# Optimization experiments

Hardware: AMD Instinct MI355X
Metric: run time of the kernel (lower is better)

The kernel has to match this reference:

```python
import jax, jax.numpy as jnp
import numpy as np

EPS = 1e-12  # F.normalize default eps


def setup_inputs() -> dict:
    key = jax.random.key(0)
    x = jax.random.normal(key, (10000, 512), dtype=jnp.float32)
    return {"x": x, "k": 9}


def reference(x, k):
    # F.normalize(x, p=2, dim=0): L2-normalize each feature column over points
    col_norm = jnp.sqrt(jnp.sum(x * x, axis=0, keepdims=True))  # [1, D]
    xn = x / jnp.maximum(col_norm, EPS)                          # [N, D]

    # pairwise squared euclidean distance: ||xi||^2 - 2 xi.xj + ||xj||^2
    sq = jnp.sum(xn * xn, axis=-1, keepdims=True)                # [N, 1]
    dist = sq - 2.0 * (xn @ xn.T) + sq.T                          # [N, N]

    # k nearest neighbors = top-k of negative distance
    _, nn_idx = jax.lax.top_k(-dist, k)                           # [N, k] int32

    n = x.shape[0]
    center_idx = jnp.broadcast_to(jnp.arange(n, dtype=nn_idx.dtype)[:, None], (n, k))
    edge_idx = jnp.stack((nn_idx, center_idx), axis=0)            # [2, N, k]
    return edge_idx
```

## Files before the change

kernel.cpp:

```cpp
#include <hip/hip_runtime.h>
#include <hip/hip_cooperative_groups.h>
#include <math.h>

namespace cg = cooperative_groups;

#define DD 512
#define NBLKA 400

#define PM 128
#define PN 256
#define KB 32
#define CSPLIT 6
#define NC 12
#define PBUF 32
#define PBSTRIDE 36
#define NCTOT (CSPLIT*NC)
#define KOUTMAX 16
#define RS_MARGIN 2e-4f

typedef __attribute__((ext_vector_type(8))) short bf16x8;
typedef __attribute__((ext_vector_type(4))) float f32x4;

static __device__ __forceinline__ unsigned short f2bf(float f) {
    unsigned u = __float_as_uint(f);
    u += 0x7fff + ((u >> 16) & 1);
    return (unsigned short)(u >> 16);
}

__global__ __launch_bounds__(256) void prekernel(
    const float* __restrict__ x, double* __restrict__ partial,
    double* __restrict__ rn, double* __restrict__ w,
    double* __restrict__ sq, float* __restrict__ sqf,
    unsigned short* __restrict__ xnbf, int N, int rows_per_block, int nblk)
{
    cg::grid_group grid = cg::this_grid();
    const int t = threadIdx.x;

    {
        int b  = blockIdx.x;
        int r0 = b * rows_per_block;
        int r1 = min(r0 + rows_per_block, N);
        double s0 = 0.0, s1 = 0.0;
        for (int r = r0; r < r1; ++r) {
            float v0 = x[(size_t)r * DD + t];
            float v1 = x[(size_t)r * DD + t + 256];
            s0 += (double)v0 * (double)v0;
            s1 += (double)v1 * (double)v1;
        }
        partial[(size_t)b * DD + t]       = s0;
        partial[(size_t)b * DD + t + 256] = s1;
    }
    grid.sync();

    __shared__ double red[256];
    if (blockIdx.x < 256) {
#pragma unroll 1
        for (int cc = 0; cc < 2; ++cc) {
            int c = blockIdx.x * 2 + cc;
            double s = 0.0;
            for (int b = t; b < nblk; b += 256) s += partial[(size_t)b * DD + c];
            red[t] = s;
            __syncthreads();
            for (int off = 128; off > 0; off >>= 1) {
                if (t < off) red[t] += red[t + off];
                __syncthreads();
            }
            if (t == 0) {
                double n = fmax(sqrt(red[0]), 1e-12);
                double r = 1.0 / n;
                rn[c] = r;
                w[c]  = r * r;
            }
            __syncthreads();
        }
    }
    grid.sync();

    {
        int lane   = t & 63;
        int gwave  = (blockIdx.x * blockDim.x + t) >> 6;
        int nwaves = (gridDim.x * blockDim.x) >> 6;
        const double2* rp = (const double2*)rn;
        double2 r0a = rp[lane * 2],       r0b = rp[lane * 2 + 1];
        double2 r1a = rp[128 + lane * 2], r1b = rp[128 + lane * 2 + 1];
        for (int i = gwave; i < N; i += nwaves) {
            const float4* xr = (const float4*)(x + (size_t)i * DD);
            float4 v0 = xr[lane];
            float4 v1 = xr[64 + lane];
            double a0 = (double)v0.x * r0a.x, a1 = (double)v0.y * r0a.y;
            double a2 = (double)v0.z * r0b.x, a3 = (double)v0.w * r0b.y;
            double b0 = (double)v1.x * r1a.x, b1 = (double)v1.y * r1a.y;
            double b2 = (double)v1.z * r1b.x, b3 = (double)v1.w * r1b.y;
            ushort4 s0 = { f2bf((float)a0), f2bf((float)a1), f2bf((float)a2), f2bf((float)a3) };
            ushort4 s1 = { f2bf((float)b0), f2bf((float)b1), f2bf((float)b2), f2bf((float)b3) };
            *(ushort4*)(xnbf + (size_t)i * DD + lane * 4)       = s0;
            *(ushort4*)(xnbf + (size_t)i * DD + 256 + lane * 4) = s1;
            double loc = a0*a0 + a1*a1 + a2*a2 + a3*a3 + b0*b0 + b1*b1 + b2*b2 + b3*b3;
#pragma unroll
            for (int off = 32; off > 0; off >>= 1)
                loc += __shfl_xor(loc, off, 64);
            if (lane == 0) { sq[i] = loc; sqf[i] = (float)loc; }
        }
    }
}

__global__ __launch_bounds__(512, 2) void gemm_dummy_guard() {}

__global__ __launch_bounds__(256, 2) void gemm_prefilter(
    const unsigned short* __restrict__ xnbf,
    const float* __restrict__ sqf, int* __restrict__ cand, float* __restrict__ cands,
    int N, int ntileM, int ntileN)
{
    __shared__ __align__(16) unsigned char lds_raw[49152];
    __shared__ float sqi_s[PM];
    __shared__ float sqj_s[PN];
    __shared__ float thr_s[PM];
    __shared__ int   cnt_s[PM];
    __shared__ int   flag_s;

    float (*Bsc)[PBSTRIDE] = (float (*)[PBSTRIDE]) lds_raw;
    int   (*Bid)[PBSTRIDE] = (int   (*)[PBSTRIDE]) (lds_raw + 24576);

    const int bid   = blockIdx.x;
    const int q     = bid & 7;
    const int s     = bid >> 3;
    const int ridx  = s / CSPLIT;
    const int split = s - ridx * CSPLIT;
    const int rowb  = q + 8 * ridx;
    if (rowb >= ntileM) return;
    const int row0  = rowb * PM;

    const int t      = threadIdx.x;
    const int lane15 = t & 15;
    const int quad   = (t >> 4) & 3;
    const int wave   = t >> 6;
    const int wr     = (wave >> 1) * 64;
    const int wc     = (wave & 1) * 128;
    const int sl     = quad ^ (lane15 & 3);

    if (t == 0) flag_s = 0;
    if (t < PM) {
        int i = row0 + t;
        sqi_s[t] = (i < N) ? sqf[i] : 0.f;
        thr_s[t] = __builtin_inff();
        cnt_s[t] = 0;
    }

    float ls[NC];
    int   li[NC];
#pragma unroll
    for (int m = 0; m < NC; ++m) { ls[m] = __builtin_inff(); li[m] = 0x7fffffff; }

    f32x4 acc[4][8];

    for (int tile = split; tile < ntileN; tile += CSPLIT) {
        int col0 = tile * PN;

        {
            int j = col0 + t;
            sqj_s[t] = (j < N) ? sqf[j] : __builtin_inff();
        }
        __syncthreads();

#pragma unroll
        for (int mt = 0; mt < 4; ++mt)
#pragma unroll
            for (int nt = 0; nt < 8; ++nt)
                acc[mt][nt] = (f32x4){0.f, 0.f, 0.f, 0.f};

        auto STAGE = [&](int kc, int buf) {
            unsigned char* base = lds_raw + (size_t)buf * 24576;
#pragma unroll
            for (int l = 0; l < 2; ++l) {
                int e   = t + l * 256;
                int row = e >> 2;
                int c   = (e & 3) ^ (row & 3);
                size_t g = (size_t)(row0 + row) * DD + kc + c * 8;
                __builtin_amdgcn_global_load_lds(
                    (const unsigned int*)(xnbf + g),
                    (unsigned int*)(base + (size_t)e * 16), 16, 0, 0);
            }
#pragma unroll
            for (int l = 0; l < 4; ++l) {
                int e   = t + l * 256;
                int row = e >> 2;
                int c   = (e & 3) ^ (row & 3);
                size_t g = (size_t)(col0 + row) * DD + kc + c * 8;
                __builtin_amdgcn_global_load_lds(
                    (const unsigned int*)(xnbf + g),
                    (unsigned int*)(base + 8192 + (size_t)e * 16), 16, 0, 0);
            }
        };

        STAGE(0, 0);
#pragma unroll 1
        for (int cc = 0; cc < 16; ++cc) {
            if (cc < 15) {
                STAGE((cc + 1) * KB, (cc + 1) & 1);
                __builtin_amdgcn_sched_barrier(0);
                asm volatile("s_waitcnt vmcnt(6)" ::: "memory");
            } else {
                __builtin_amdgcn_sched_barrier(0);
                asm volatile("s_waitcnt vmcnt(0)" ::: "memory");
            }
            __builtin_amdgcn_s_barrier();
            __builtin_amdgcn_sched_barrier(0);

            const unsigned char* rb = lds_raw + (size_t)(cc & 1) * 24576;
            bf16x8 af[4], bfg[8];
#pragma unroll
            for (int mt = 0; mt < 4; ++mt)
                af[mt] = *(const bf16x8*)(rb + (size_t)(wr + mt * 16 + lane15) * 64 + sl * 16);
#pragma unroll
            for (int nt = 0; nt < 8; ++nt)
                bfg[nt] = *(const bf16x8*)(rb + 8192 + (size_t)(wc + nt * 16 + lane15) * 64 + sl * 16);
#pragma unroll
            for (int mt = 0; mt < 4; ++mt)
#pragma unroll
                for (int nt = 0; nt < 8; ++nt)
                    acc[mt][nt] = __builtin_amdgcn_mfma_f32_16x16x32_bf16(
                        af[mt], bfg[nt], acc[mt][nt], 0, 0, 0);
            __builtin_amdgcn_sched_barrier(0);
            __builtin_amdgcn_s_barrier();
        }

#pragma unroll
        for (int mt = 0; mt < 4; ++mt)
#pragma unroll
            for (int nt = 0; nt < 8; ++nt)
#pragma unroll
                for (int reg = 0; reg < 4; ++reg) {
                    int rl = wr + mt * 16 + quad * 4 + reg;
                    int cl = wc + nt * 16 + lane15;
                    float g = acc[mt][nt][reg];
                    acc[mt][nt][reg] = (sqi_s[rl] - 2.f * g) + sqj_s[cl];
                }
        __syncthreads();

        bool tile_edge = (col0 + PN > N);
        unsigned long long done0 = 0ull, done1 = 0ull;
        for (;;) {
#pragma unroll
            for (int hn = 0; hn < 2; ++hn) {
#pragma unroll
                for (int mt = 0; mt < 4; ++mt)
#pragma unroll
                    for (int reg = 0; reg < 4; ++reg) {
                        const unsigned long long gb =
                            (0x1111ull << reg) << (mt * 16);
                        unsigned long long dn = hn ? done1 : done0;
                        int rl = wr + mt * 16 + quad * 4 + reg;
                        float th = thr_s[rl];
                        float gmin = fminf(
                            fminf(acc[mt][hn * 4 + 0][reg], acc[mt][hn * 4 + 1][reg]),
                            fminf(acc[mt][hn * 4 + 2][reg], acc[mt][hn * 4 + 3][reg]));
                        if (!tile_edge && gmin > th) {
                            if (hn) done1 |= gb; else done0 |= gb;
                            continue;
                        }
                        if ((dn & gb) == gb) continue;
#pragma unroll
                        for (int u = 0; u < 4; ++u) {
                            const unsigned long long bit = 1ull << (mt * 16 + u * 4 + reg);
                            if (!(dn & bit)) {
                                float sv = acc[mt][hn * 4 + u][reg];
                                int   j  = col0 + wc + (hn * 4 + u) * 16 + lane15;
                                bool ok = false;
                                if (j < N && sv <= th) {
                                    int pos = atomicAdd(&cnt_s[rl], 1);
                                    if (pos < PBUF) {
                                        Bsc[rl][pos] = sv;
                                        Bid[rl][pos] = j;
                                        ok = true;
                                    }
                                } else {
                                    ok = true;
                                }
                                if (ok) { if (hn) done1 |= bit; else done0 |= bit; }
                            }
                        }
                    }
            }
            if (done0 != ~0ull || done1 != ~0ull) flag_s = 1;
            __syncthreads();
            if (t < PM) {
                int c = cnt_s[t];
                if (c > PBUF) c = PBUF;
                cnt_s[t] = 0;
                for (int m0 = 0; m0 < c; m0 += 4) {
                    float4 s4 = *(const float4*)&Bsc[t][m0];
                    int4   j4 = *(const int4*)&Bid[t][m0];
#pragma unroll
                    for (int e = 0; e < 4; ++e) {
                        if (m0 + e >= c) break;
                        float sv = (e == 0) ? s4.x : (e == 1) ? s4.y : (e == 2) ? s4.z : s4.w;
                        int   j  = (e == 0) ? j4.x : (e == 1) ? j4.y : (e == 2) ? j4.z : j4.w;
                        if (sv < ls[NC - 1] || (sv == ls[NC - 1] && j < li[NC - 1])) {
                            float cs = sv; int cj = j;
#pragma unroll
                            for (int p = 0; p < NC; ++p) {
                                bool lt = (cs < ls[p]) || (cs == ls[p] && cj < li[p]);
                                float ts = ls[p]; int tj = li[p];
                                if (lt) { ls[p] = cs; li[p] = cj; cs = ts; cj = tj; }
                            }
                        }
                    }
                }
                thr_s[t] = ls[NC - 1];
            }
            __syncthreads();
            int go = flag_s;
            __syncthreads();
            if (t == 0) flag_s = 0;
            __syncthreads();
            if (!go) break;
        }
    }
    if (t < PM) {
        int i = row0 + t;
        if (i < N) {
#pragma unroll
            for (int m = 0; m < NC; ++m) {
                cand [(size_t)i * NCTOT + split * NC + m] = li[m];
                cands[(size_t)i * NCTOT + split * NC + m] = ls[m];
            }
        }
    }
}

__global__ __launch_bounds__(256) void rescore_topk(
    const float* __restrict__ x, const double* __restrict__ w,
    const double* __restrict__ sq, const int* __restrict__ cand,
    const float* __restrict__ cands, int* __restrict__ out, int N, int k)
{
    __shared__ float Ssc[4][NCTOT];
    int lane = threadIdx.x & 63;
    int wid  = threadIdx.x >> 6;
    int i = blockIdx.x * 4 + wid;
    if (i >= N) return;

    size_t base = (size_t)i * NCTOT;
    Ssc[wid][lane] = cands[base + lane];
    if (lane < NCTOT - 64) Ssc[wid][64 + lane] = cands[base + 64 + lane];

    float p0 = Ssc[wid][lane];
    float p1 = Ssc[wid][64 + (lane & 7)];
    int c0 = 0, c1 = 0;
    for (int m = 0; m < NCTOT; ++m) {
        float s = Ssc[wid][m];
        c0 += (s <= p0); c1 += (s <= p1);
    }
    float best = __builtin_inff();
    if (c0 >= k) best = p0;
    if (c1 >= k && p1 < best) best = p1;
#pragma unroll
    for (int off = 32; off > 0; off >>= 1)
        best = fminf(best, __shfl_xor(best, off, 64));
    float cut = best + RS_MARGIN;

    double aw[8];
#pragma unroll
    for (int c = 0; c < 8; ++c) {
        int d = lane + 64 * c;
        aw[c] = (double)x[(size_t)i * DD + d] * w[d];
    }
    double sqi = sq[i];

    double bs[KOUTMAX];
    int    bj[KOUTMAX];
    for (int r = 0; r < k; ++r) { bs[r] = __builtin_inf(); bj[r] = 0x7fffffff; }

    int pend = -1;
    for (int m = 0; m <= NCTOT; ++m) {
        int j1cand = -1;
        if (m < NCTOT) {
            if (Ssc[wid][m] > cut) continue;
            j1cand = cand[base + m];
            if (pend < 0) { pend = j1cand; continue; }
        } else if (pend < 0) {
            break;
        }
        int j0 = pend, j1 = j1cand;
        pend = -1;
        const float* q0 = &x[(size_t)j0 * DD + lane];
        const float* q1 = (j1 >= 0) ? &x[(size_t)j1 * DD + lane] : q0;
        float v0[8], v1[8];
#pragma unroll
        for (int c = 0; c < 8; ++c) v0[c] = q0[64 * c];
#pragma unroll
        for (int c = 0; c < 8; ++c) v1[c] = q1[64 * c];
        double d0 = 0.0, d1 = 0.0;
#pragma unroll
        for (int c = 0; c < 8; ++c) d0 = fma(aw[c], (double)v0[c], d0);
#pragma unroll
        for (int c = 0; c < 8; ++c) d1 = fma(aw[c], (double)v1[c], d1);
#pragma unroll
        for (int off = 32; off > 0; off >>= 1) {
            d0 += __shfl_xor(d0, off, 64);
            d1 += __shfl_xor(d1, off, 64);
        }
        double s0 = (sqi - 2.0 * d0) + sq[j0];
        double s1 = (j1 >= 0) ? (sqi - 2.0 * d1) + sq[j1] : __builtin_inf();
#pragma unroll 1
        for (int pick = 0; pick < 2; ++pick) {
            double sv = pick ? s1 : s0;
            int    j  = pick ? j1 : j0;
            if (j < 0) continue;
            if (sv < bs[k - 1] || (sv == bs[k - 1] && j < bj[k - 1])) {
                int pos = k - 1;
                while (pos > 0) {
                    double ps = bs[pos - 1]; int pj = bj[pos - 1];
                    if (!(sv < ps || (sv == ps && j < pj))) break;
                    bs[pos] = ps; bj[pos] = pj;
                    --pos;
                }
                bs[pos] = sv; bj[pos] = j;
            }
        }
    }
    if (lane == 0) {
        for (int r = 0; r < k; ++r) {
            out[(size_t)i * k + r]                 = bj[r];
            out[(size_t)N * k + (size_t)i * k + r] = i;
        }
    }
}

extern "C" void kernel_launch(void* const* d_in, const int* in_sizes, int n_in,
                              void* d_out, int out_size, void* d_ws, size_t ws_size,
                              hipStream_t stream) {
    const float* x = (const float*)d_in[0];
    int N = in_sizes[0] / DD;
    int k = out_size / (2 * N);
    if (k > KOUTMAX) k = KOUTMAX;

    char* ws = (char*)d_ws;
    double*         partial = (double*)ws;
    double*         rn      = (double*)(ws + 1638400);
    double*         w       = (double*)(ws + 1642496);
    double*         sq      = (double*)(ws + 1646592);
    float*          sqf     = (float*) (ws + 1726592);
    unsigned short* xnbf    = (unsigned short*)(ws + 1766592);
    int*            cand    = (int*)   (ws + 12006592);
    float*          cands   = (float*) (ws + 14886592);

    int rpb  = (N + NBLKA - 1) / NBLKA;
    int nblk = NBLKA;
    void* pre_args[] = { (void*)&x, (void*)&partial, (void*)&rn, (void*)&w,
                         (void*)&sq, (void*)&sqf, (void*)&xnbf,
                         (void*)&N, (void*)&rpb, (void*)&nblk };
    hipLaunchCooperativeKernel((const void*)prekernel, dim3(NBLKA), dim3(256),
                               pre_args, 0, stream);

    int ntileM = (N + PM - 1) / PM;
    int ntileN = (N + PN - 1) / PN;
    int rows_per_xcd = (ntileM + 7) / 8;
    int nblkc = 8 * rows_per_xcd * CSPLIT;
    hipLaunchKernelGGL(gemm_prefilter, dim3(nblkc), dim3(256), 0, stream,
                       xnbf, sqf, cand, cands, N, ntileM, ntileN);

    hipLaunchKernelGGL(rescore_topk, dim3((N + 3) / 4), dim3(256), 0, stream,
                       x, w, sq, cand, cands, (int*)d_out, N, k);
}
```

Before: 712.1 us.

## Switch prefilter GEMM from bf16 to scaled fp8 MFMA with wider candidate set

Normalized features are quantized to e4m3 fp8 (scaled by 32) instead of bf16, and the prefilter GEMM uses the fp8 16x16x32 MFMA with K-chunks of 32 bytes, halving staging traffic and LDS use. Per-split candidate count rises from 12 to 16 and the rescoring margin widens to absorb the larger fp8 error. The rescore also applies a dynamic cut based on the current k-th best exact distance, so fewer candidates get rescored. The trade-off is more candidates to rescore and a higher risk of missing a true neighbor if fp8 error exceeds the margin.

```diff
diff --git a/kernel.cpp b/kernel.cpp
--- a/kernel.cpp
+++ b/kernel.cpp
@@ -11,27 +11,56 @@
 #define PN 256
 #define KB 32
 #define CSPLIT 6
-#define NC 12
+#define NC 16
 #define PBUF 32
 #define PBSTRIDE 36
 #define NCTOT (CSPLIT*NC)
 #define KOUTMAX 16
-#define RS_MARGIN 2e-4f
-
-typedef __attribute__((ext_vector_type(8))) short bf16x8;
+#define RS_MARGIN 3e-3f
+#define DYN_MARGIN 1.5e-3f
+#define FP8SCALE 32.f
+#define INVS2 (1.f/512.f)
+
 typedef __attribute__((ext_vector_type(4))) float f32x4;
 
-static __device__ __forceinline__ unsigned short f2bf(float f) {
+static __device__ __forceinline__ unsigned char f2e4m3(float f) {
     unsigned u = __float_as_uint(f);
-    u += 0x7fff + ((u >> 16) & 1);
-    return (unsigned short)(u >> 16);
+    unsigned sgn = (u >> 24) & 0x80;
+    int e = (int)((u >> 23) & 0xff);
+    unsigned m = u & 0x7fffff;
+    int te = e - 120;
+    unsigned r;
+    if (te >= 1) {
+        unsigned mm   = m >> 20;
+        unsigned rest = m & 0xfffff;
+        if (rest > 0x80000 || (rest == 0x80000 && (mm & 1))) ++mm;
+        if (mm == 8) { mm = 0; ++te; }
+        if (te > 15 || (te == 15 && mm == 7)) r = 0x7e;
+        else r = (unsigned)((te << 3) | mm);
+    } else {
+        int sh = 1 - te;
+        if (sh > 24 || e == 0) r = 0;
+        else {
+            unsigned full = m | 0x800000;
+            int sa = 20 + sh;
+            if (sa > 31) r = 0;
+            else {
+                unsigned shifted = full >> sa;
+                unsigned rem  = full & ((1u << sa) - 1);
+                unsigned half = 1u << (sa - 1);
+                if (rem > half || (rem == half && (shifted & 1))) ++shifted;
+                r = shifted;
+            }
+        }
+    }
+    return (unsigned char)(r | sgn);
 }
 
 __global__ __launch_bounds__(256) void prekernel(
     const float* __restrict__ x, double* __restrict__ partial,
     double* __restrict__ rn, double* __restrict__ w,
     double* __restrict__ sq, float* __restrict__ sqf,
-    unsigned short* __restrict__ xnbf, int N, int rows_per_block, int nblk)
+    unsigned char* __restrict__ xnbf8, int N, int rows_per_block, int nblk)
 {
     cg::grid_group grid = cg::this_grid();
     const int t = threadIdx.x;
@@ -91,10 +120,12 @@
             double a2 = (double)v0.z * r0b.x, a3 = (double)v0.w * r0b.y;
             double b0 = (double)v1.x * r1a.x, b1 = (double)v1.y * r1a.y;
             double b2 = (double)v1.z * r1b.x, b3 = (double)v1.w * r1b.y;
-            ushort4 s0 = { f2bf((float)a0), f2bf((float)a1), f2bf((float)a2), f2bf((float)a3) };
-            ushort4 s1 = { f2bf((float)b0), f2bf((float)b1), f2bf((float)b2), f2bf((float)b3) };
-            *(ushort4*)(xnbf + (size_t)i * DD + lane * 4)       = s0;
-            *(ushort4*)(xnbf + (size_t)i * DD + 256 + lane * 4) = s1;
+            uchar4 c0 = { f2e4m3(FP8SCALE * (float)a0), f2e4m3(FP8SCALE * (float)a1),
+                          f2e4m3(FP8SCALE * (float)a2), f2e4m3(FP8SCALE * (float)a3) };
+            uchar4 c1 = { f2e4m3(FP8SCALE * (float)b0), f2e4m3(FP8SCALE * (float)b1),
+                          f2e4m3(FP8SCALE * (float)b2), f2e4m3(FP8SCALE * (float)b3) };
+            *(uchar4*)(xnbf8 + (size_t)i * DD + lane * 4)       = c0;
+            *(uchar4*)(xnbf8 + (size_t)i * DD + 256 + lane * 4) = c1;
             double loc = a0*a0 + a1*a1 + a2*a2 + a3*a3 + b0*b0 + b1*b1 + b2*b2 + b3*b3;
 #pragma unroll
             for (int off = 32; off > 0; off >>= 1)
@@ -104,22 +135,19 @@
     }
 }
 
-__global__ __launch_bounds__(512, 2) void gemm_dummy_guard() {}
-
 __global__ __launch_bounds__(256, 2) void gemm_prefilter(
-    const unsigned short* __restrict__ xnbf,
+    const unsigned char* __restrict__ xnbf8,
     const float* __restrict__ sqf, int* __restrict__ cand, float* __restrict__ cands,
     int N, int ntileM, int ntileN)
 {
-    __shared__ __align__(16) unsigned char lds_raw[49152];
+    __shared__ __align__(16) unsigned char lds_raw[24576];
+    __shared__ __align__(16) float Bsc[PM][PBSTRIDE];
+    __shared__ __align__(16) int   Bid[PM][PBSTRIDE];
     __shared__ float sqi_s[PM];
     __shared__ float sqj_s[PN];
     __shared__ float thr_s[PM];
     __shared__ int   cnt_s[PM];
     __shared__ int   flag_s;
-
-    float (*Bsc)[PBSTRIDE] = (float (*)[PBSTRIDE]) lds_raw;
-    int   (*Bid)[PBSTRIDE] = (int   (*)[PBSTRIDE]) (lds_raw + 24576);
 
     const int bid   = blockIdx.x;
     const int q     = bid & 7;
@@ -136,7 +164,8 @@
     const int wave   = t >> 6;
     const int wr     = (wave >> 1) * 64;
     const int wc     = (wave & 1) * 128;
-    const int sl     = quad ^ (lane15 & 3);
+    const int ag     = quad >> 1;
+    const int asub   = (quad & 1) * 8;
 
     if (t == 0) flag_s = 0;
     if (t < PM) {
@@ -169,26 +198,25 @@
                 acc[mt][nt] = (f32x4){0.f, 0.f, 0.f, 0.f};
 
         auto STAGE = [&](int kc, int buf) {
-            unsigned char* base = lds_raw + (size_t)buf * 24576;
+            unsigned char* base = lds_raw + (size_t)buf * 12288;
+            {
+                int e   = t;
+                int row = e >> 1;
+                int c   = (e & 1) ^ (row & 1);
+                size_t g = (size_t)(row0 + row) * DD + kc + c * 16;
+                __builtin_amdgcn_global_load_lds(
+                    (const unsigned int*)(xnbf8 + g),
+                    (unsigned int*)(base + (size_t)e * 16), 16, 0, 0);
+            }
 #pragma unroll
             for (int l = 0; l < 2; ++l) {
                 int e   = t + l * 256;
-                int row = e >> 2;
-                int c   = (e & 3) ^ (row & 3);
-                size_t g = (size_t)(row0 + row) * DD + kc + c * 8;
+                int row = e >> 1;
+                int c   = (e & 1) ^ (row & 1);
+                size_t g = (size_t)(col0 + row) * DD + kc + c * 16;
                 __builtin_amdgcn_global_load_lds(
-                    (const unsigned int*)(xnbf + g),
-                    (unsigned int*)(base + (size_t)e * 16), 16, 0, 0);
-            }
-#pragma unroll
-            for (int l = 0; l < 4; ++l) {
-                int e   = t + l * 256;
-                int row = e >> 2;
-                int c   = (e & 3) ^ (row & 3);
-                size_t g = (size_t)(col0 + row) * DD + kc + c * 8;
-                __builtin_amdgcn_global_load_lds(
-                    (const unsigned int*)(xnbf + g),
-                    (unsigned int*)(base + 8192 + (size_t)e * 16), 16, 0, 0);
+                    (const unsigned int*)(xnbf8 + g),
+                    (unsigned int*)(base + 4096 + (size_t)e * 16), 16, 0, 0);
             }
         };
 
@@ -198,7 +226,7 @@
             if (cc < 15) {
                 STAGE((cc + 1) * KB, (cc + 1) & 1);
                 __builtin_amdgcn_sched_barrier(0);
-                asm volatile("s_waitcnt vmcnt(6)" ::: "memory");
+                asm volatile("s_waitcnt vmcnt(3)" ::: "memory");
             } else {
                 __builtin_amdgcn_sched_barrier(0);
                 asm volatile("s_waitcnt vmcnt(0)" ::: "memory");
@@ -206,19 +234,23 @@
             __builtin_amdgcn_s_barrier();
             __builtin_amdgcn_sched_barrier(0);
 
-            const unsigned char* rb = lds_raw + (size_t)(cc & 1) * 24576;
-            bf16x8 af[4], bfg[8];
+            const unsigned char* rb = lds_raw + (size_t)(cc & 1) * 12288;
+            long af[4], bfg[8];
+#pragma unroll
+            for (int mt = 0; mt < 4; ++mt) {
+                int row = wr + mt * 16 + lane15;
+                af[mt] = *(const long*)(rb + (size_t)row * 32 + (size_t)(ag ^ (row & 1)) * 16 + asub);
+            }
+#pragma unroll
+            for (int nt = 0; nt < 8; ++nt) {
+                int row = wc + nt * 16 + lane15;
+                bfg[nt] = *(const long*)(rb + 4096 + (size_t)row * 32 + (size_t)(ag ^ (row & 1)) * 16 + asub);
+            }
 #pragma unroll
             for (int mt = 0; mt < 4; ++mt)
-                af[mt] = *(const bf16x8*)(rb + (size_t)(wr + mt * 16 + lane15) * 64 + sl * 16);
-#pragma unroll
-            for (int nt = 0; nt < 8; ++nt)
-                bfg[nt] = *(const bf16x8*)(rb + 8192 + (size_t)(wc + nt * 16 + lane15) * 64 + sl * 16);
-#pragma unroll
-            for (int mt = 0; mt < 4; ++mt)
 #pragma unroll
                 for (int nt = 0; nt < 8; ++nt)
-                    acc[mt][nt] = __builtin_amdgcn_mfma_f32_16x16x32_bf16(
+                    acc[mt][nt] = __builtin_amdgcn_mfma_f32_16x16x32_fp8_fp8(
                         af[mt], bfg[nt], acc[mt][nt], 0, 0, 0);
             __builtin_amdgcn_sched_barrier(0);
             __builtin_amdgcn_s_barrier();
@@ -233,7 +265,7 @@
                     int rl = wr + mt * 16 + quad * 4 + reg;
                     int cl = wc + nt * 16 + lane15;
                     float g = acc[mt][nt][reg];
-                    acc[mt][nt][reg] = (sqi_s[rl] - 2.f * g) + sqj_s[cl];
+                    acc[mt][nt][reg] = fmaf(-INVS2, g, sqi_s[rl] + sqj_s[cl]);
                 }
         __syncthreads();
 
@@ -344,7 +376,7 @@
     if (lane < NCTOT - 64) Ssc[wid][64 + lane] = cands[base + 64 + lane];
 
     float p0 = Ssc[wid][lane];
-    float p1 = Ssc[wid][64 + (lane & 7)];
+    float p1 = Ssc[wid][64 + (lane & 31)];
     int c0 = 0, c1 = 0;
     for (int m = 0; m < NCTOT; ++m) {
         float s = Ssc[wid][m];
@@ -374,7 +406,8 @@
     for (int m = 0; m <= NCTOT; ++m) {
         int j1cand = -1;
         if (m < NCTOT) {
-            if (Ssc[wid][m] > cut) continue;
+            float dcut = fminf(cut, (float)bs[k - 1] + DYN_MARGIN);
+            if (Ssc[wid][m] > dcut) continue;
             j1cand = cand[base + m];
             if (pend < 0) { pend = j1cand; continue; }
         } else if (pend < 0) {
@@ -435,19 +468,19 @@
     if (k > KOUTMAX) k = KOUTMAX;
 
     char* ws = (char*)d_ws;
-    double*         partial = (double*)ws;
-    double*         rn      = (double*)(ws + 1638400);
-    double*         w       = (double*)(ws + 1642496);
-    double*         sq      = (double*)(ws + 1646592);
-    float*          sqf     = (float*) (ws + 1726592);
-    unsigned short* xnbf    = (unsigned short*)(ws + 1766592);
-    int*            cand    = (int*)   (ws + 12006592);
-    float*          cands   = (float*) (ws + 14886592);
+    double*        partial = (double*)ws;
+    double*        rn      = (double*)(ws + 1638400);
+    double*        w       = (double*)(ws + 1642496);
+    double*        sq      = (double*)(ws + 1646592);
+    float*         sqf     = (float*) (ws + 1726592);
+    unsigned char* xnbf8   = (unsigned char*)(ws + 1766592);
+    int*           cand    = (int*)   (ws + 6886592);
+    float*         cands   = (float*) (ws + 10726592);
 
     int rpb  = (N + NBLKA - 1) / NBLKA;
     int nblk = NBLKA;
     void* pre_args[] = { (void*)&x, (void*)&partial, (void*)&rn, (void*)&w,
-                         (void*)&sq, (void*)&sqf, (void*)&xnbf,
+                         (void*)&sq, (void*)&sqf, (void*)&xnbf8,
                          (void*)&N, (void*)&rpb, (void*)&nblk };
     hipLaunchCooperativeKernel((const void*)prekernel, dim3(NBLKA), dim3(256),
                                pre_args, 0, stream);
@@ -457,7 +490,7 @@
     int rows_per_xcd = (ntileM + 7) / 8;
     int nblkc = 8 * rows_per_xcd * CSPLIT;
     hipLaunchKernelGGL(gemm_prefilter, dim3(nblkc), dim3(256), 0, stream,
-                       xnbf, sqf, cand, cands, N, ntileM, ntileN);
+                       xnbf8, sqf, cand, cands, N, ntileM, ntileN);
 
     hipLaunchKernelGGL(rescore_topk, dim3((N + 3) / 4), dim3(256), 0, stream,
                        x, w, sq, cand, cands, (int*)d_out, N, k);
```

Result: slower. 959.5 us (+34.7%).
